# Kernel tuning notes

Measured on AMD Instinct MI355X. Metric: run time of the kernel, lower is better.

The kernel has to match this reference:

```python
import jax, jax.numpy as jnp
import numpy as np

B, C, F, H, W = 4, 256, 16, 32, 32


def setup_inputs() -> dict:
    key = jax.random.key(0)
    ks = jax.random.split(key, 8)
    x = jax.random.normal(ks[0], (B, C, F, H, W), dtype=jnp.float32)
    wq = jax.random.normal(ks[1], (C, C), dtype=jnp.float32) * 0.05
    bq = jax.random.normal(ks[2], (C,), dtype=jnp.float32) * 0.05
    wk = jax.random.normal(ks[3], (C, C), dtype=jnp.float32) * 0.05
    bk = jax.random.normal(ks[4], (C,), dtype=jnp.float32) * 0.05
    wv = jax.random.normal(ks[5], (C, C), dtype=jnp.float32) * 0.05
    bv = jax.random.normal(ks[6], (C,), dtype=jnp.float32) * 0.05
    gamma = jax.random.normal(ks[7], (1,), dtype=jnp.float32) * 0.1
    return {"x": x, "wq": wq, "bq": bq, "wk": wk, "bk": bk, "wv": wv, "bv": bv, "gamma": gamma}


def reference(x, wq, bq, wk, bk, wv, bv, gamma):
    b, c, f, h, w = x.shape
    p = h * w
    # replicate torch .view(batch*frames, channels, H, W): raw memory reinterpretation
    xr = x.reshape(b * f, c, p)  # [B*F, C, HW]
    proj = lambda wt, bi: jnp.einsum('ncp,dc->ndp', xr, wt) + bi[None, :, None]
    q = proj(wq, bq).reshape(b, f, c, p).transpose(0, 2, 1, 3)  # [B, C, F, HW]
    k = proj(wk, bk).reshape(b, f, c, p).transpose(0, 2, 3, 1)  # [B, C, HW, F]
    v = proj(wv, bv).reshape(b, f, c, p).transpose(0, 2, 1, 3)  # [B, C, F, HW]
    attn = jax.nn.softmax(jnp.matmul(q, k) * (1.0 / c ** 0.5), axis=-1)  # [B, C, F, F]
    out = jnp.matmul(attn, v)  # [B, C, F, HW]
    # replicate permute(0,2,1,3).view(B,F,C,H,W).permute(0,2,1,3,4)
    out = out.transpose(0, 2, 1, 3).reshape(b, f, c, h, w).transpose(0, 2, 1, 3, 4)
    return gamma * out + x
```

## Files before the change

### kernel.cpp

```cpp
#include <hip/hip_runtime.h>
#include <hip/hip_bf16.h>

#define CC 256
#define FF 16
#define PP 1024
#define BB 4
#define NN 64

typedef __bf16 bf16x8 __attribute__((ext_vector_type(8)));
typedef float  f32x4  __attribute__((ext_vector_type(4)));

__device__ __forceinline__ void async16(const __hip_bfloat16* g, char* l) {
    __builtin_amdgcn_global_load_lds(
        (const __attribute__((address_space(1))) unsigned int*)g,
        (__attribute__((address_space(3))) unsigned int*)l, 16, 0, 0);
}

__device__ __forceinline__ float bf2f(unsigned short u) {
    union { unsigned i; float f; } v; v.i = ((unsigned)u) << 16; return v.f;
}

__global__ __launch_bounds__(256) void xt_kernel(
    const float* __restrict__ x,
    const float* __restrict__ wq, const float* __restrict__ wk,
    const float* __restrict__ wv,
    __hip_bfloat16* __restrict__ Xt, __hip_bfloat16* __restrict__ Wb)
{
    __shared__ float T[64][65];
    const int n = blockIdx.z;
    const int t = threadIdx.x;

    if (n == NN) {
        const int blk = blockIdx.y * 16 + blockIdx.x;
        const int idx = (blk * 256 + t) * 4;
        #pragma unroll
        for (int proj = 0; proj < 3; ++proj) {
            const float* src = proj == 0 ? wq : (proj == 1 ? wk : wv);
            __hip_bfloat16* dst = Wb + (size_t)proj * CC * CC;
            const float4 v = *(const float4*)(src + idx);
            __hip_bfloat162 h0, h1;
            h0.x = __float2bfloat16(v.x); h0.y = __float2bfloat16(v.y);
            h1.x = __float2bfloat16(v.z); h1.y = __float2bfloat16(v.w);
            *(__hip_bfloat162*)(dst + idx)     = h0;
            *(__hip_bfloat162*)(dst + idx + 2) = h1;
        }
        return;
    }

    const int c0 = blockIdx.y * 64, p0 = blockIdx.x * 64;
    const int pl = t & 63, r0 = t >> 6;
    const float* xp = x + ((size_t)n * CC + c0) * PP + p0;
    #pragma unroll
    for (int i = 0; i < 16; ++i) {
        const int cl = r0 + i * 4;
        T[cl][pl] = xp[(size_t)cl * PP + pl];
    }
    __syncthreads();
    __hip_bfloat16* op = Xt + ((size_t)n * PP + p0) * CC + c0;
    const int cl2 = (t & 31) * 2, q0 = t >> 5;
    #pragma unroll
    for (int j = 0; j < 8; ++j) {
        const int pr = q0 + j * 8;
        __hip_bfloat162 h;
        h.x = __float2bfloat16(T[cl2][pr]);
        h.y = __float2bfloat16(T[cl2 + 1][pr]);
        *(__hip_bfloat162*)(op + (size_t)pr * CC + cl2) = h;
    }
}

__global__ __launch_bounds__(256) void qkv_mfma(
    const __hip_bfloat16* __restrict__ Wb, const __hip_bfloat16* __restrict__ Xt,
    const float* __restrict__ bq, const float* __restrict__ bk,
    const float* __restrict__ bv,
    __hip_bfloat16* __restrict__ Qw, __hip_bfloat16* __restrict__ Kw,
    __hip_bfloat16* __restrict__ Vw)
{
    __shared__ char lds[36864];

    const int p0 = blockIdx.x * 128, d0 = blockIdx.y * 128;
    const int z = blockIdx.z, proj = z % 3, n = z / 3;
    const int t = threadIdx.x, w = t >> 6, lane = t & 63;
    const int wd = (w >> 1) * 64, wp = (w & 1) * 64;
    const int q = lane >> 4, m16 = lane & 15;

    const __hip_bfloat16* Abase = Wb + (size_t)proj * CC * CC + (size_t)d0 * CC;
    const __hip_bfloat16* Bbase = Xt + (size_t)n * PP * CC + (size_t)p0 * CC;

    f32x4 acc[4][4];
    #pragma unroll
    for (int i = 0; i < 4; ++i)
        #pragma unroll
        for (int j = 0; j < 4; ++j)
            acc[i][j] = (f32x4){0.f, 0.f, 0.f, 0.f};

    for (int c0 = 0; c0 < CC; c0 += 64) {
        #pragma unroll
        for (int k = 0; k < 4; ++k) {
            const int s = t + 256 * k;
            const int row = s >> 3;
            const int gc = (s & 7) ^ (row & 7);
            async16(Abase + (size_t)row * CC + c0 + gc * 8, lds + s * 16);
            async16(Bbase + (size_t)row * CC + c0 + gc * 8, lds + 16384 + s * 16);
        }
        __syncthreads();
        #pragma unroll
        for (int kk = 0; kk < 2; ++kk) {
            bf16x8 a[4], b[4];
            #pragma unroll
            for (int i = 0; i < 4; ++i) {
                const int row = wd + i * 16 + m16;
                const int col = (4 * kk + q) ^ (row & 7);
                a[i] = *(const bf16x8*)(lds + row * 128 + col * 16);
            }
            #pragma unroll
            for (int j = 0; j < 4; ++j) {
                const int row = wp + j * 16 + m16;
                const int col = (4 * kk + q) ^ (row & 7);
                b[j] = *(const bf16x8*)(lds + 16384 + row * 128 + col * 16);
            }
            #pragma unroll
            for (int i = 0; i < 4; ++i)
                #pragma unroll
                for (int j = 0; j < 4; ++j)
                    acc[i][j] = __builtin_amdgcn_mfma_f32_16x16x32_bf16(a[i], b[j], acc[i][j], 0, 0, 0);
        }
        __syncthreads();
    }

    __syncthreads();
    char* wb = lds + w * 9216;
    const int dl2 = lane >> 3, pl2 = lane & 7;

    const float* bias = (proj == 0) ? bq : ((proj == 1) ? bk : bv);
    #pragma unroll
    for (int i = 0; i < 4; ++i)
        #pragma unroll
        for (int r = 0; r < 4; ++r) {
            const int d_l = i * 16 + q * 4 + r;
            const float bb = bias[d0 + wd + d_l];
            #pragma unroll
            for (int j = 0; j < 4; ++j) {
                const int p_l = j * 16 + m16;
                *(__hip_bfloat16*)(wb + d_l * 144 + p_l * 2) =
                    __float2bfloat16(acc[i][j][r] + bb);
            }
        }

    __hip_bfloat16* dst;
    size_t dstride;
    if (proj < 2) {
        dst = ((proj == 0) ? Qw : Kw) + (size_t)n * CC * PP
              + (size_t)(d0 + wd) * PP + p0 + wp;
        dstride = PP;
    } else {
        const int b = n >> 4, f = n & 15;
        dst = Vw + (((size_t)(b * CC + d0 + wd)) * FF + f) * PP + p0 + wp;
        dstride = (size_t)FF * PP;
    }
    #pragma unroll
    for (int k = 0; k < 8; ++k) {
        const int d_l = k * 8 + dl2;
        bf16x8 v = *(const bf16x8*)(wb + d_l * 144 + pl2 * 16);
        *(bf16x8*)(dst + (size_t)d_l * dstride + pl2 * 8) = v;
    }
}

__global__ __launch_bounds__(256) void attn_out(
    const __hip_bfloat16* __restrict__ Qw, const __hip_bfloat16* __restrict__ Kw,
    const __hip_bfloat16* __restrict__ Vw,
    const float* __restrict__ x, const float* __restrict__ gamma,
    float* __restrict__ out)
{
    const int d = blockIdx.x, b = blockIdx.y;
    const int t = threadIdx.x, w = t >> 6, lane = t & 63;
    const int q = lane >> 4, m16 = lane & 15;
    __shared__ float Sp[4][16][17];
    __shared__ float As[16][17];

    {
        const size_t gbase = ((size_t)(b * 16 + m16) * CC + d) * PP + w * 256 + q * 8;
        f32x4 acc0 = {0.f, 0.f, 0.f, 0.f}, acc1 = {0.f, 0.f, 0.f, 0.f};
        #pragma unroll
        for (int pc = 0; pc < 256; pc += 64) {
            bf16x8 aq0 = *(const bf16x8*)(Qw + gbase + pc);
            bf16x8 bk0 = *(const bf16x8*)(Kw + gbase + pc);
            bf16x8 aq1 = *(const bf16x8*)(Qw + gbase + pc + 32);
            bf16x8 bk1 = *(const bf16x8*)(Kw + gbase + pc + 32);
            acc0 = __builtin_amdgcn_mfma_f32_16x16x32_bf16(aq0, bk0, acc0, 0, 0, 0);
            acc1 = __builtin_amdgcn_mfma_f32_16x16x32_bf16(aq1, bk1, acc1, 0, 0, 0);
        }
        #pragma unroll
        for (int r = 0; r < 4; ++r)
            Sp[w][q * 4 + r][m16] = acc0[r] + acc1[r];
    }
    __syncthreads();

    {
        const int f1 = t >> 4, f2 = t & 15;
        const float s = (Sp[0][f1][f2] + Sp[1][f1][f2] + Sp[2][f1][f2] + Sp[3][f1][f2]) * 0.0625f;
        float m = s;
        #pragma unroll
        for (int off = 1; off < 16; off <<= 1) m = fmaxf(m, __shfl_xor(m, off));
        const float e = __expf(s - m);
        float den = e;
        #pragma unroll
        for (int off = 1; off < 16; off <<= 1) den += __shfl_xor(den, off);
        As[f1][f2] = e / den;
    }
    __syncthreads();

    const float g = gamma[0];
    const size_t base = ((size_t)(b * CC + d) * FF) * PP + t * 4;
    const __hip_bfloat16* Vb = Vw + base;
    f32x4 vv[16];
    #pragma unroll
    for (int f2 = 0; f2 < 16; ++f2) {
        const ushort4 rv = *(const ushort4*)(Vb + (size_t)f2 * PP);
        vv[f2] = (f32x4){ bf2f(rv.x), bf2f(rv.y), bf2f(rv.z), bf2f(rv.w) };
    }
    #pragma unroll
    for (int f1 = 0; f1 < 16; ++f1) {
        f32x4 a = {0.f, 0.f, 0.f, 0.f};
        #pragma unroll
        for (int f2 = 0; f2 < 16; ++f2) {
            const float av = As[f1][f2];
            a += av * vv[f2];
        }
        const f32x4 xv = *(const f32x4*)(x + base + (size_t)f1 * PP);
        const f32x4 res = g * a + xv;
        *(f32x4*)(out + base + (size_t)f1 * PP) = res;
    }
}

extern "C" void kernel_launch(void* const* d_in, const int* in_sizes, int n_in,
                              void* d_out, int out_size, void* d_ws, size_t ws_size,
                              hipStream_t stream) {
    const float* x     = (const float*)d_in[0];
    const float* wq    = (const float*)d_in[1];
    const float* bq    = (const float*)d_in[2];
    const float* wk    = (const float*)d_in[3];
    const float* bk    = (const float*)d_in[4];
    const float* wv    = (const float*)d_in[5];
    const float* bv    = (const float*)d_in[6];
    const float* gamma = (const float*)d_in[7];
    float* out = (float*)d_out;

    __hip_bfloat16* Qw = (__hip_bfloat16*)d_ws;
    __hip_bfloat16* Kw = Qw + (size_t)NN * CC * PP;
    __hip_bfloat16* Vw = Kw + (size_t)NN * CC * PP;
    __hip_bfloat16* Wb = Vw + (size_t)NN * CC * PP;
    __hip_bfloat16* Xt = (__hip_bfloat16*)d_out;

    xt_kernel<<<dim3(PP / 64, CC / 64, NN + 1), 256, 0, stream>>>(
        x, wq, wk, wv, Xt, Wb);
    qkv_mfma<<<dim3(PP / 128, CC / 128, NN * 3), 256, 0, stream>>>(
        Wb, Xt, bq, bk, bv, Qw, Kw, Vw);
    attn_out<<<dim3(CC, BB), 256, 0, stream>>>(Qw, Kw, Vw, x, gamma, out);
}
```

Before: 192.5 us.

## Fuse Q/K/V projections into one block sharing the X tile

Each qkv_mfma block now computes all three projections for its (p, d) tile. It loads the three weight tiles and one shared X tile into a 64KB LDS buffer, and the grid is cut to one third. This removes the redundant loading of the same X tile by three separate blocks and lets one B fragment feed three sets of MFMAs. In exchange, each thread holds three times as many accumulators, and both register pressure and LDS use per block rise, which may limit occupancy despite launch_bounds(256,2).

```diff
diff --git a/kernel.cpp b/kernel.cpp
--- a/kernel.cpp
+++ b/kernel.cpp
@@ -68,30 +68,34 @@
     }
 }
 
-__global__ __launch_bounds__(256) void qkv_mfma(
+__global__ __launch_bounds__(256, 2) void qkv_mfma(
     const __hip_bfloat16* __restrict__ Wb, const __hip_bfloat16* __restrict__ Xt,
     const float* __restrict__ bq, const float* __restrict__ bk,
     const float* __restrict__ bv,
     __hip_bfloat16* __restrict__ Qw, __hip_bfloat16* __restrict__ Kw,
     __hip_bfloat16* __restrict__ Vw)
 {
-    __shared__ char lds[36864];
+    __shared__ char lds[65536];
 
     const int p0 = blockIdx.x * 128, d0 = blockIdx.y * 128;
-    const int z = blockIdx.z, proj = z % 3, n = z / 3;
+    const int n = blockIdx.z;
     const int t = threadIdx.x, w = t >> 6, lane = t & 63;
     const int wd = (w >> 1) * 64, wp = (w & 1) * 64;
     const int q = lane >> 4, m16 = lane & 15;
 
-    const __hip_bfloat16* Abase = Wb + (size_t)proj * CC * CC + (size_t)d0 * CC;
+    const __hip_bfloat16* Aq = Wb + (size_t)d0 * CC;
+    const __hip_bfloat16* Ak = Aq + (size_t)CC * CC;
+    const __hip_bfloat16* Av = Ak + (size_t)CC * CC;
     const __hip_bfloat16* Bbase = Xt + (size_t)n * PP * CC + (size_t)p0 * CC;
 
-    f32x4 acc[4][4];
-    #pragma unroll
-    for (int i = 0; i < 4; ++i)
-        #pragma unroll
-        for (int j = 0; j < 4; ++j)
-            acc[i][j] = (f32x4){0.f, 0.f, 0.f, 0.f};
+    f32x4 acc[3][4][4];
+    #pragma unroll
+    for (int pr = 0; pr < 3; ++pr)
+        #pragma unroll
+        for (int i = 0; i < 4; ++i)
+            #pragma unroll
+            for (int j = 0; j < 4; ++j)
+                acc[pr][i][j] = (f32x4){0.f, 0.f, 0.f, 0.f};
 
     for (int c0 = 0; c0 < CC; c0 += 64) {
         #pragma unroll
@@ -99,69 +103,79 @@
             const int s = t + 256 * k;
             const int row = s >> 3;
             const int gc = (s & 7) ^ (row & 7);
-            async16(Abase + (size_t)row * CC + c0 + gc * 8, lds + s * 16);
-            async16(Bbase + (size_t)row * CC + c0 + gc * 8, lds + 16384 + s * 16);
+            const size_t goff = (size_t)row * CC + c0 + gc * 8;
+            async16(Aq + goff,    lds +         s * 16);
+            async16(Ak + goff,    lds + 16384 + s * 16);
+            async16(Av + goff,    lds + 32768 + s * 16);
+            async16(Bbase + goff, lds + 49152 + s * 16);
         }
         __syncthreads();
         #pragma unroll
         for (int kk = 0; kk < 2; ++kk) {
-            bf16x8 a[4], b[4];
-            #pragma unroll
-            for (int i = 0; i < 4; ++i) {
-                const int row = wd + i * 16 + m16;
-                const int col = (4 * kk + q) ^ (row & 7);
-                a[i] = *(const bf16x8*)(lds + row * 128 + col * 16);
-            }
+            bf16x8 b[4];
             #pragma unroll
             for (int j = 0; j < 4; ++j) {
                 const int row = wp + j * 16 + m16;
                 const int col = (4 * kk + q) ^ (row & 7);
-                b[j] = *(const bf16x8*)(lds + 16384 + row * 128 + col * 16);
+                b[j] = *(const bf16x8*)(lds + 49152 + row * 128 + col * 16);
             }
             #pragma unroll
-            for (int i = 0; i < 4; ++i)
+            for (int proj = 0; proj < 3; ++proj) {
+                bf16x8 a[4];
                 #pragma unroll
-                for (int j = 0; j < 4; ++j)
-                    acc[i][j] = __builtin_amdgcn_mfma_f32_16x16x32_bf16(a[i], b[j], acc[i][j], 0, 0, 0);
+                for (int i = 0; i < 4; ++i) {
+                    const int row = wd + i * 16 + m16;
+                    const int col = (4 * kk + q) ^ (row & 7);
+                    a[i] = *(const bf16x8*)(lds + proj * 16384 + row * 128 + col * 16);
+                }
+                #pragma unroll
+                for (int i = 0; i < 4; ++i)
+                    #pragma unroll
+                    for (int j = 0; j < 4; ++j)
+                        acc[proj][i][j] = __builtin_amdgcn_mfma_f32_16x16x32_bf16(
+                            a[i], b[j], acc[proj][i][j], 0, 0, 0);
+            }
         }
         __syncthreads();
     }
 
-    __syncthreads();
     char* wb = lds + w * 9216;
     const int dl2 = lane >> 3, pl2 = lane & 7;
 
-    const float* bias = (proj == 0) ? bq : ((proj == 1) ? bk : bv);
-    #pragma unroll
-    for (int i = 0; i < 4; ++i)
-        #pragma unroll
-        for (int r = 0; r < 4; ++r) {
-            const int d_l = i * 16 + q * 4 + r;
-            const float bb = bias[d0 + wd + d_l];
-            #pragma unroll
-            for (int j = 0; j < 4; ++j) {
-                const int p_l = j * 16 + m16;
-                *(__hip_bfloat16*)(wb + d_l * 144 + p_l * 2) =
-                    __float2bfloat16(acc[i][j][r] + bb);
+    #pragma unroll
+    for (int proj = 0; proj < 3; ++proj) {
+        const float* bias = (proj == 0) ? bq : ((proj == 1) ? bk : bv);
+        #pragma unroll
+        for (int i = 0; i < 4; ++i)
+            #pragma unroll
+            for (int r = 0; r < 4; ++r) {
+                const int d_l = i * 16 + q * 4 + r;
+                const float bb = bias[d0 + wd + d_l];
+                #pragma unroll
+                for (int j = 0; j < 4; ++j) {
+                    const int p_l = j * 16 + m16;
+                    *(__hip_bfloat16*)(wb + d_l * 144 + p_l * 2) =
+                        __float2bfloat16(acc[proj][i][j][r] + bb);
+                }
             }
-        }
-
-    __hip_bfloat16* dst;
-    size_t dstride;
-    if (proj < 2) {
-        dst = ((proj == 0) ? Qw : Kw) + (size_t)n * CC * PP
-              + (size_t)(d0 + wd) * PP + p0 + wp;
-        dstride = PP;
-    } else {
-        const int b = n >> 4, f = n & 15;
-        dst = Vw + (((size_t)(b * CC + d0 + wd)) * FF + f) * PP + p0 + wp;
-        dstride = (size_t)FF * PP;
-    }
-    #pragma unroll
-    for (int k = 0; k < 8; ++k) {
-        const int d_l = k * 8 + dl2;
-        bf16x8 v = *(const bf16x8*)(wb + d_l * 144 + pl2 * 16);
-        *(bf16x8*)(dst + (size_t)d_l * dstride + pl2 * 8) = v;
+
+        __hip_bfloat16* dst;
+        size_t dstride;
+        if (proj < 2) {
+            dst = ((proj == 0) ? Qw : Kw) + (size_t)n * CC * PP
+                  + (size_t)(d0 + wd) * PP + p0 + wp;
+            dstride = PP;
+        } else {
+            const int b = n >> 4, f = n & 15;
+            dst = Vw + (((size_t)(b * CC + d0 + wd)) * FF + f) * PP + p0 + wp;
+            dstride = (size_t)FF * PP;
+        }
+        #pragma unroll
+        for (int k = 0; k < 8; ++k) {
+            const int d_l = k * 8 + dl2;
+            bf16x8 v = *(const bf16x8*)(wb + d_l * 144 + pl2 * 16);
+            *(bf16x8*)(dst + (size_t)d_l * dstride + pl2 * 8) = v;
+        }
     }
 }
 
@@ -253,7 +267,7 @@
 
     xt_kernel<<<dim3(PP / 64, CC / 64, NN + 1), 256, 0, stream>>>(
         x, wq, wk, wv, Xt, Wb);
-    qkv_mfma<<<dim3(PP / 128, CC / 128, NN * 3), 256, 0, stream>>>(
+    qkv_mfma<<<dim3(PP / 128, CC / 128, NN), 256, 0, stream>>>(
         Wb, Xt, bq, bk, bv, Qw, Kw, Vw);
     attn_out<<<dim3(CC, BB), 256, 0, stream>>>(Qw, Kw, Vw, x, gamma, out);
 }
```

After: 216.4 us. 12.4% more time.

## Double-buffer LDS tiles in QKV projection GEMM with async prefetch

Applied to the files above, without the earlier changes.

Makes the QKV projection GEMM use two LDS buffers. The next 64-wide K slice is issued as async global-to-LDS loads while MFMAs run on the current one, with explicit vmcnt waits and barriers instead of full __syncthreads. The epilogue is also split into Q/K and V branches, each with its own store stride. LDS use per block grows from 36KB to 64KB, which may lower occupancy.

```diff
diff --git a/kernel.cpp b/kernel.cpp
--- a/kernel.cpp
+++ b/kernel.cpp
@@ -75,7 +75,7 @@
     __hip_bfloat16* __restrict__ Qw, __hip_bfloat16* __restrict__ Kw,
     __hip_bfloat16* __restrict__ Vw)
 {
-    __shared__ char lds[36864];
+    __shared__ char lds[65536];
 
     const int p0 = blockIdx.x * 128, d0 = blockIdx.y * 128;
     const int z = blockIdx.z, proj = z % 3, n = z / 3;
@@ -93,16 +93,31 @@
         for (int j = 0; j < 4; ++j)
             acc[i][j] = (f32x4){0.f, 0.f, 0.f, 0.f};
 
-    for (int c0 = 0; c0 < CC; c0 += 64) {
+    auto stage = [&](int bo, int c0) {
         #pragma unroll
         for (int k = 0; k < 4; ++k) {
             const int s = t + 256 * k;
             const int row = s >> 3;
             const int gc = (s & 7) ^ (row & 7);
-            async16(Abase + (size_t)row * CC + c0 + gc * 8, lds + s * 16);
-            async16(Bbase + (size_t)row * CC + c0 + gc * 8, lds + 16384 + s * 16);
-        }
-        __syncthreads();
+            const size_t goff = (size_t)row * CC + c0 + gc * 8;
+            async16(Abase + goff, lds + bo + s * 16);
+            async16(Bbase + goff, lds + bo + 16384 + s * 16);
+        }
+    };
+
+    stage(0, 0);
+    #pragma unroll
+    for (int step = 0; step < 4; ++step) {
+        const int bo = (step & 1) * 32768;
+        if (step < 3) {
+            stage(32768 - bo, (step + 1) * 64);
+            asm volatile("s_waitcnt vmcnt(8)" ::: "memory");
+        } else {
+            asm volatile("s_waitcnt vmcnt(0)" ::: "memory");
+        }
+        __builtin_amdgcn_sched_barrier(0);
+        __builtin_amdgcn_s_barrier();
+
         #pragma unroll
         for (int kk = 0; kk < 2; ++kk) {
             bf16x8 a[4], b[4];
@@ -110,13 +125,13 @@
             for (int i = 0; i < 4; ++i) {
                 const int row = wd + i * 16 + m16;
                 const int col = (4 * kk + q) ^ (row & 7);
-                a[i] = *(const bf16x8*)(lds + row * 128 + col * 16);
+                a[i] = *(const bf16x8*)(lds + bo + row * 128 + col * 16);
             }
             #pragma unroll
             for (int j = 0; j < 4; ++j) {
                 const int row = wp + j * 16 + m16;
                 const int col = (4 * kk + q) ^ (row & 7);
-                b[j] = *(const bf16x8*)(lds + 16384 + row * 128 + col * 16);
+                b[j] = *(const bf16x8*)(lds + bo + 16384 + row * 128 + col * 16);
             }
             #pragma unroll
             for (int i = 0; i < 4; ++i)
@@ -124,44 +139,56 @@
                 for (int j = 0; j < 4; ++j)
                     acc[i][j] = __builtin_amdgcn_mfma_f32_16x16x32_bf16(a[i], b[j], acc[i][j], 0, 0, 0);
         }
-        __syncthreads();
-    }
-
-    __syncthreads();
+        __builtin_amdgcn_s_barrier();
+    }
+
     char* wb = lds + w * 9216;
     const int dl2 = lane >> 3, pl2 = lane & 7;
 
-    const float* bias = (proj == 0) ? bq : ((proj == 1) ? bk : bv);
-    #pragma unroll
-    for (int i = 0; i < 4; ++i)
-        #pragma unroll
-        for (int r = 0; r < 4; ++r) {
-            const int d_l = i * 16 + q * 4 + r;
-            const float bb = bias[d0 + wd + d_l];
-            #pragma unroll
-            for (int j = 0; j < 4; ++j) {
-                const int p_l = j * 16 + m16;
-                *(__hip_bfloat16*)(wb + d_l * 144 + p_l * 2) =
-                    __float2bfloat16(acc[i][j][r] + bb);
-            }
-        }
-
-    __hip_bfloat16* dst;
-    size_t dstride;
     if (proj < 2) {
-        dst = ((proj == 0) ? Qw : Kw) + (size_t)n * CC * PP
-              + (size_t)(d0 + wd) * PP + p0 + wp;
-        dstride = PP;
+        const float* bias = (proj == 0) ? bq : bk;
+        #pragma unroll
+        for (int i = 0; i < 4; ++i)
+            #pragma unroll
+            for (int r = 0; r < 4; ++r) {
+                const int d_l = i * 16 + q * 4 + r;
+                const float bb = bias[d0 + wd + d_l];
+                #pragma unroll
+                for (int j = 0; j < 4; ++j) {
+                    const int p_l = j * 16 + m16;
+                    *(__hip_bfloat16*)(wb + d_l * 144 + p_l * 2) =
+                        __float2bfloat16(acc[i][j][r] + bb);
+                }
+            }
+        __hip_bfloat16* dst = ((proj == 0) ? Qw : Kw) + (size_t)n * CC * PP;
+        #pragma unroll
+        for (int k = 0; k < 8; ++k) {
+            const int d_l = k * 8 + dl2;
+            bf16x8 v = *(const bf16x8*)(wb + d_l * 144 + pl2 * 16);
+            *(bf16x8*)(dst + (size_t)(d0 + wd + d_l) * PP + p0 + wp + pl2 * 8) = v;
+        }
     } else {
+        #pragma unroll
+        for (int i = 0; i < 4; ++i)
+            #pragma unroll
+            for (int r = 0; r < 4; ++r) {
+                const int d_l = i * 16 + q * 4 + r;
+                const float bb = bv[d0 + wd + d_l];
+                #pragma unroll
+                for (int j = 0; j < 4; ++j) {
+                    const int p_l = j * 16 + m16;
+                    *(__hip_bfloat16*)(wb + d_l * 144 + p_l * 2) =
+                        __float2bfloat16(acc[i][j][r] + bb);
+                }
+            }
         const int b = n >> 4, f = n & 15;
-        dst = Vw + (((size_t)(b * CC + d0 + wd)) * FF + f) * PP + p0 + wp;
-        dstride = (size_t)FF * PP;
-    }
-    #pragma unroll
-    for (int k = 0; k < 8; ++k) {
-        const int d_l = k * 8 + dl2;
-        bf16x8 v = *(const bf16x8*)(wb + d_l * 144 + pl2 * 16);
-        *(bf16x8*)(dst + (size_t)d_l * dstride + pl2 * 8) = v;
+        __hip_bfloat16* dst = Vw + (((size_t)(b * CC + d0 + wd)) * FF + f) * PP + p0 + wp;
+        #pragma unroll
+        for (int k = 0; k < 8; ++k) {
+            const int d_l = k * 8 + dl2;
+            bf16x8 v = *(const bf16x8*)(wb + d_l * 144 + pl2 * 16);
+            *(bf16x8*)(dst + (size_t)d_l * FF * PP + pl2 * 8) = v;
+        }
     }
 }
 
```

Result: no change. 194.0 us (+0.8%).
